# Kernel tuning notes

Measured on AMD Instinct MI355X. Metric: run time of the kernel, lower is better.

## Reference

```python
import jax, jax.numpy as jnp
import numpy as np

H = 16          # num heads
DH = 64         # head size
D = H * DH      # hidden size 1024
B, S = 2, 2048


def setup_inputs() -> dict:
    key = jax.random.key(0)
    ks = jax.random.split(key, 9)
    scale = 1.0 / np.sqrt(D)
    p = {}
    p["hidden_states"] = jax.random.normal(ks[0], (B, S, D), dtype=jnp.float32)
    for i, name in enumerate(["q", "k", "v", "o"]):
        # stored so that y = x @ W + b (transpose of torch Linear weight)
        p[f"W{name}"] = jax.random.normal(ks[1 + 2 * i], (D, D), dtype=jnp.float32) * scale
        p[f"b{name}"] = jax.random.normal(ks[2 + 2 * i], (D,), dtype=jnp.float32) * 0.01
    return p


def reference(hidden_states, Wq, bq, Wk, bk, Wv, bv, Wo, bo):
    b, s, _ = hidden_states.shape
    q = hidden_states @ Wq + bq  # [B,S,D]
    k = hidden_states @ Wk + bk
    v = hidden_states @ Wv + bv
    # [B,H,S,DH]
    q = q.reshape(b, s, H, DH).transpose(0, 2, 1, 3)
    k = k.reshape(b, s, H, DH).transpose(0, 2, 1, 3)
    v = v.reshape(b, s, H, DH).transpose(0, 2, 1, 3)
    scores = jnp.einsum("bhqd,bhkd->bhqk", q, k) / np.sqrt(DH)
    causal = jnp.triu(jnp.ones((s, s), dtype=bool), k=1)  # True above diagonal -> masked
    scores = jnp.where(causal, -jnp.inf, scores)
    attn = jax.nn.softmax(scores, axis=-1)  # dropout p=0 (eval)
    ctx = jnp.einsum("bhqk,bhkd->bhqd", attn, v)
    ctx = ctx.transpose(0, 2, 1, 3).reshape(b, s, D)
    return ctx @ Wo + bo
```

## Files before the change

kernel.cpp:

```cpp
#include <hip/hip_runtime.h>


typedef _Float16 f16x8 __attribute__((ext_vector_type(8)));
typedef _Float16 f16x4 __attribute__((ext_vector_type(4)));
typedef __fp16 h16x2 __attribute__((ext_vector_type(2)));
typedef float f32x4 __attribute__((ext_vector_type(4)));
typedef float f32x16 __attribute__((ext_vector_type(16)));

#define GLD_LDS16(g, l)                                                        \
  __builtin_amdgcn_global_load_lds(                                            \
      (__attribute__((address_space(1))) const unsigned int*)(g),              \
      (__attribute__((address_space(3))) unsigned int*)(l), 16, 0, 0)

static constexpr int Sdim = 2048;
static constexpr int Ddim = 1024;
static constexpr int NH = 16;
static constexpr int DH = 64;
static constexpr int Mrows = 4096;

static constexpr float QSCALE = 0.125f * 1.44269504f;

__global__ __launch_bounds__(256) void xcvt(const float* __restrict__ X,
                                            _Float16* __restrict__ Y) {
  size_t i = ((size_t)blockIdx.x * 256 + threadIdx.x) * 8;
  float4 f0 = *(const float4*)(X + i);
  float4 f1 = *(const float4*)(X + i + 4);
  alignas(16) _Float16 h[8] = {(_Float16)f0.x, (_Float16)f0.y, (_Float16)f0.z,
                               (_Float16)f0.w, (_Float16)f1.x, (_Float16)f1.y,
                               (_Float16)f1.z, (_Float16)f1.w};
  *(uint4*)(Y + i) = *(const uint4*)h;
}

struct WtArgs {
  const float *s0, *s1, *s2, *s3;
  _Float16 *d0, *d1, *d2, *d3;
};

__global__ __launch_bounds__(256) void wtrans(WtArgs a) {
  __shared__ _Float16 L[64 * 72];
  const int z = blockIdx.z;
  const float* src = z == 0 ? a.s0 : z == 1 ? a.s1 : z == 2 ? a.s2 : a.s3;
  _Float16* dst = z == 0 ? a.d0 : z == 1 ? a.d1 : z == 2 ? a.d2 : a.d3;
  const int k0 = blockIdx.x * 64, n0 = blockIdx.y * 64, t = threadIdx.x;
#pragma unroll
  for (int i = 0; i < 4; ++i) {
    int c = i * 256 + t;
    int row = c >> 4, cc = c & 15;
    float4 f = *(const float4*)&src[(size_t)(k0 + row) * Ddim + n0 + cc * 4];
    L[(cc * 4 + 0) * 72 + row] = (_Float16)f.x;
    L[(cc * 4 + 1) * 72 + row] = (_Float16)f.y;
    L[(cc * 4 + 2) * 72 + row] = (_Float16)f.z;
    L[(cc * 4 + 3) * 72 + row] = (_Float16)f.w;
  }
  __syncthreads();
#pragma unroll
  for (int i = 0; i < 2; ++i) {
    int c = i * 256 + t;
    int n = c >> 3, cc = c & 7;
    *(uint4*)&dst[(size_t)(n0 + n) * Ddim + k0 + cc * 8] =
        *(const uint4*)&L[n * 72 + cc * 8];
  }
}

struct GemmArgs {
  const _Float16* A;
  const _Float16 *Bt0, *Bt1, *Bt2;
  const float *b0, *b1, *b2;
  void *o0, *o1, *o2;
};

template <int MODE>
__global__ __launch_bounds__(256) void gemm128(GemmArgs g) {
  constexpr int K = 1024;
  __shared__ _Float16 As[128 * 32];
  __shared__ _Float16 Bs[128 * 32];
  const int z = blockIdx.z;
  const _Float16* A = g.A;
  const _Float16* Bt = z == 0 ? g.Bt0 : z == 1 ? g.Bt1 : g.Bt2;
  const float* bias = z == 0 ? g.b0 : z == 1 ? g.b1 : g.b2;
  void* out = z == 0 ? g.o0 : z == 1 ? g.o1 : g.o2;
  const int m0 = blockIdx.x * 128, n0 = blockIdx.y * 128;
  const int t = threadIdx.x, lane = t & 63, wv = t >> 6;
  const int wm = wv >> 1, wn = wv & 1, quad = lane >> 4, r = lane & 15;

  const int c0 = wv * 64 + lane, c1 = c0 + 256;
  const _Float16* ga0 = A + (size_t)(m0 + (c0 >> 2)) * K + (c0 & 3) * 8;
  const _Float16* ga1 = A + (size_t)(m0 + (c1 >> 2)) * K + (c1 & 3) * 8;
  const _Float16* gb0 = Bt + (size_t)(n0 + (c0 >> 2)) * K + (c0 & 3) * 8;
  const _Float16* gb1 = Bt + (size_t)(n0 + (c1 >> 2)) * K + (c1 & 3) * 8;
  char* lA0 = (char*)As + (wv * 64) * 16;
  char* lA1 = (char*)As + (256 + wv * 64) * 16;
  char* lB0 = (char*)Bs + (wv * 64) * 16;
  char* lB1 = (char*)Bs + (256 + wv * 64) * 16;

  f32x4 acc[4][4] = {};
  for (int kt = 0; kt < K; kt += 32) {
    GLD_LDS16(ga0 + kt, lA0);
    GLD_LDS16(ga1 + kt, lA1);
    GLD_LDS16(gb0 + kt, lB0);
    GLD_LDS16(gb1 + kt, lB1);
    __syncthreads();
    f16x8 af[4], bf[4];
#pragma unroll
    for (int mi = 0; mi < 4; ++mi)
      af[mi] = *(const f16x8*)&As[(wm * 64 + mi * 16 + r) * 32 + quad * 8];
#pragma unroll
    for (int ni = 0; ni < 4; ++ni)
      bf[ni] = *(const f16x8*)&Bs[(wn * 64 + ni * 16 + r) * 32 + quad * 8];
#pragma unroll
    for (int mi = 0; mi < 4; ++mi)
#pragma unroll
      for (int ni = 0; ni < 4; ++ni)
        acc[mi][ni] = __builtin_amdgcn_mfma_f32_16x16x32_f16(af[mi], bf[ni],
                                                             acc[mi][ni], 0, 0, 0);
    __syncthreads();
  }

  const float scale = (MODE == 0 && z == 0) ? QSCALE : 1.0f;
  float bv[4];
#pragma unroll
  for (int ni = 0; ni < 4; ++ni) bv[ni] = bias[n0 + wn * 64 + ni * 16 + r];
#pragma unroll
  for (int mi = 0; mi < 4; ++mi) {
#pragma unroll
    for (int ni = 0; ni < 4; ++ni) {
      const int n = n0 + wn * 64 + ni * 16 + r;
      if (MODE == 0 && z == 2) {
        alignas(8) _Float16 h4[4];
#pragma unroll
        for (int reg = 0; reg < 4; ++reg)
          h4[reg] = (_Float16)(acc[mi][ni][reg] + bv[ni]);
        const int m = m0 + wm * 64 + mi * 16 + quad * 4;
        const int b = m >> 11, s = m & 2047, h = n >> 6, dh = n & 63;
        *(uint2*)&((_Float16*)out)[((size_t)(b * NH + h) * DH + dh) * Sdim + s] =
            *(const uint2*)h4;
      } else {
#pragma unroll
        for (int reg = 0; reg < 4; ++reg) {
          const int m = m0 + wm * 64 + mi * 16 + quad * 4 + reg;
          const float v = (acc[mi][ni][reg] + bv[ni]) * scale;
          if (MODE == 0) {
            const int b = m >> 11, s = m & 2047, h = n >> 6, dh = n & 63;
            ((_Float16*)out)[(((size_t)(b * NH + h) * Sdim + s) << 6) + dh] =
                (_Float16)v;
          } else {
            ((float*)out)[(size_t)m * Ddim + n] = v;
          }
        }
      }
    }
  }
}

__global__ __launch_bounds__(256) void attn(const _Float16* __restrict__ Q,
                                            const _Float16* __restrict__ Kk,
                                            const _Float16* __restrict__ Vt,
                                            _Float16* __restrict__ ctx) {
  __shared__ _Float16 Ks[2][64 * 64], Vs[2][64 * 64];
  const int id = blockIdx.x, xcd = id & 7, slot = id >> 3;
  const int qt = 31 - (slot >> 2);
  const int bh = ((slot & 3) << 3) | xcd;
  const int q0 = qt * 64;
  const int t = threadIdx.x, lane = t & 63, wv = t >> 6;
  const int qh = wv & 1, kvh = wv >> 1;
  const int n31 = lane & 31, h5 = lane >> 5, h8 = h5 * 8;
  const int b = bh >> 4, h = bh & 15;
  const _Float16* Kg = Kk + (size_t)bh * Sdim * DH;
  const _Float16* Vg = Vt + (size_t)bh * DH * Sdim;

  const int qg = q0 + qh * 32 + n31;
  const _Float16* Qrow = Q + ((size_t)bh * Sdim + qg) * DH;
  f16x8 aq[4];
#pragma unroll
  for (int ks = 0; ks < 4; ++ks) aq[ks] = *(const f16x8*)(Qrow + ks * 16 + h8);

  const int ntiles = qt + 1;
  const int sr = t >> 3, sr2 = sr + 32, sc = (t & 7) * 8;
  const int kr = (sr & 51) | ((sr & 4) << 1) | ((sr & 8) >> 1);
  const int kr2 = (sr2 & 51) | ((sr2 & 4) << 1) | ((sr2 & 8) >> 1);
  const int kc = sc ^ ((kr & 7) << 3), kc2 = sc ^ ((kr2 & 7) << 3);
  const int vc = sc ^ ((sr & 7) << 3), vc2 = sc ^ ((sr2 & 7) << 3);

  f32x16 oacc0 = {}, oacc1 = {};
  float l_i = 0.f;

  uint4 ka = *(const uint4*)&Kg[(size_t)sr * DH + sc];
  uint4 kb = *(const uint4*)&Kg[(size_t)sr2 * DH + sc];
  uint4 va = *(const uint4*)&Vg[(size_t)sr * Sdim + sc];
  uint4 vb = *(const uint4*)&Vg[(size_t)sr2 * Sdim + sc];
  *(uint4*)&Ks[0][kr * 64 + kc] = ka;
  *(uint4*)&Ks[0][kr2 * 64 + kc2] = kb;
  *(uint4*)&Vs[0][sr * 64 + vc] = va;
  *(uint4*)&Vs[0][sr2 * 64 + vc2] = vb;

  const int prow = kvh * 32 + n31;
  const int pb = prow * 64, psw = (prow & 7) << 3;
  const int vsw = (n31 & 7) << 3;

  for (int it = 0; it < ntiles; ++it) {
    const int cur = it & 1;
    if (it + 1 < ntiles) {
      const int kvn = (it + 1) * 64;
      ka = *(const uint4*)&Kg[(size_t)(kvn + sr) * DH + sc];
      kb = *(const uint4*)&Kg[(size_t)(kvn + sr2) * DH + sc];
      va = *(const uint4*)&Vg[(size_t)sr * Sdim + kvn + sc];
      vb = *(const uint4*)&Vg[(size_t)sr2 * Sdim + kvn + sc];
    }
    __syncthreads();

    f32x16 sacc = {};
    __builtin_amdgcn_s_setprio(1);
#pragma unroll
    for (int ks = 0; ks < 4; ++ks) {
      f16x8 ak = *(const f16x8*)&Ks[cur][pb + ((ks * 16 + h8) ^ psw)];
      sacc = __builtin_amdgcn_mfma_f32_32x32x16_f16(ak, aq[ks], sacc, 0, 0, 0);
    }
    __builtin_amdgcn_s_setprio(0);

    const int kvb = it * 64;
    if (it == ntiles - 1) {
#pragma unroll
      for (int i = 0; i < 16; ++i) {
        const int kvgl = kvb + kvh * 32 + (i & 7) + h8 + 16 * (i >> 3);
        if (kvgl > qg) sacc[i] = -1e30f;
      }
    }
#pragma unroll
    for (int i = 0; i < 16; ++i) {
      const float p = exp2f(sacc[i]);
      l_i += p;
      sacc[i] = p;
    }
    union U { f16x8 v8; h16x2 v2[4]; } u0, u1;
#pragma unroll
    for (int i = 0; i < 4; ++i) {
      u0.v2[i] = __builtin_amdgcn_cvt_pkrtz(sacc[2 * i], sacc[2 * i + 1]);
      u1.v2[i] = __builtin_amdgcn_cvt_pkrtz(sacc[8 + 2 * i], sacc[9 + 2 * i]);
    }

    __builtin_amdgcn_s_setprio(1);
#pragma unroll
    for (int ks = 0; ks < 2; ++ks) {
      const f16x8 ap = ks ? u1.v8 : u0.v8;
      const int col = kvh * 32 + ks * 16 + h8;
      f16x8 bv0 = *(const f16x8*)&Vs[cur][n31 * 64 + (col ^ vsw)];
      f16x8 bv1 = *(const f16x8*)&Vs[cur][(32 + n31) * 64 + (col ^ vsw)];
      oacc0 = __builtin_amdgcn_mfma_f32_32x32x16_f16(ap, bv0, oacc0, 0, 0, 0);
      oacc1 = __builtin_amdgcn_mfma_f32_32x32x16_f16(ap, bv1, oacc1, 0, 0, 0);
    }
    __builtin_amdgcn_s_setprio(0);

    if (it + 1 < ntiles) {
      const int nxt = cur ^ 1;
      *(uint4*)&Ks[nxt][kr * 64 + kc] = ka;
      *(uint4*)&Ks[nxt][kr2 * 64 + kc2] = kb;
      *(uint4*)&Vs[nxt][sr * 64 + vc] = va;
      *(uint4*)&Vs[nxt][sr2 * 64 + vc2] = vb;
    }
  }

  l_i += __shfl_xor(l_i, 32, 64);
  __syncthreads();
  float* obuf = (float*)&Ks[0][0] + qh * (64 * 32);
  float* lbuf = (float*)&Vs[0][0] + qh * 64;
  union V16 { f32x16 v; f32x4 q[4]; };
  if (kvh == 1) {
    V16 a, c;
    a.v = oacc0;
    c.v = oacc1;
#pragma unroll
    for (int k = 0; k < 4; ++k) {
      *(f32x4*)&obuf[lane * 32 + ((k ^ (lane & 7)) << 2)] = a.q[k];
      *(f32x4*)&obuf[lane * 32 + (((k + 4) ^ (lane & 7)) << 2)] = c.q[k];
    }
    lbuf[lane] = l_i;
  }
  __syncthreads();
  if (kvh == 0) {
    V16 a, c;
#pragma unroll
    for (int k = 0; k < 4; ++k) {
      a.q[k] = *(const f32x4*)&obuf[lane * 32 + ((k ^ (lane & 7)) << 2)];
      c.q[k] = *(const f32x4*)&obuf[lane * 32 + (((k + 4) ^ (lane & 7)) << 2)];
    }
    oacc0 += a.v;
    oacc1 += c.v;
    l_i += lbuf[lane];
#pragma unroll
    for (int rr = 0; rr < 16; ++rr) {
      const int qrow = (rr & 3) + 8 * (rr >> 2) + 4 * h5;
      const float rl = 1.0f / __shfl(l_i, qrow, 64);
      const int s = q0 + qh * 32 + qrow;
      const size_t base = ((size_t)b * Sdim + s) * Ddim + h * DH;
      ctx[base + n31] = (_Float16)(oacc0[rr] * rl);
      ctx[base + 32 + n31] = (_Float16)(oacc1[rr] * rl);
    }
  }
}

extern "C" void kernel_launch(void* const* d_in, const int* in_sizes, int n_in,
                              void* d_out, int out_size, void* d_ws,
                              size_t ws_size, hipStream_t stream) {
  const float* hid = (const float*)d_in[0];
  const float* Wq = (const float*)d_in[1];
  const float* bq = (const float*)d_in[2];
  const float* Wk = (const float*)d_in[3];
  const float* bk = (const float*)d_in[4];
  const float* Wv = (const float*)d_in[5];
  const float* bv = (const float*)d_in[6];
  const float* Wo = (const float*)d_in[7];
  const float* bo = (const float*)d_in[8];

  char* ws = (char*)d_ws;
  _Float16* Xh = (_Float16*)(ws);
  _Float16* Wqt = (_Float16*)(ws + (8ull << 20));
  _Float16* Wkt = (_Float16*)(ws + (10ull << 20));
  _Float16* Wvt = (_Float16*)(ws + (12ull << 20));
  _Float16* Wot = (_Float16*)(ws + (14ull << 20));
  _Float16* Qb = (_Float16*)(ws + (16ull << 20));
  _Float16* Kb = (_Float16*)(ws + (24ull << 20));
  _Float16* Vtb = (_Float16*)(ws + (32ull << 20));
  _Float16* ctx = Xh;

  xcvt<<<dim3(Mrows * Ddim / (256 * 8)), 256, 0, stream>>>(hid, Xh);

  WtArgs wa{Wq, Wk, Wv, Wo, Wqt, Wkt, Wvt, Wot};
  wtrans<<<dim3(16, 16, 4), 256, 0, stream>>>(wa);

  GemmArgs g1{Xh, Wqt, Wkt, Wvt, bq, bk, bv, Qb, Kb, Vtb};
  gemm128<0><<<dim3(Mrows / 128, Ddim / 128, 3), 256, 0, stream>>>(g1);

  attn<<<dim3(1024), 256, 0, stream>>>(Qb, Kb, Vtb, ctx);

  GemmArgs g2{ctx, Wot, Wot, Wot, bo, bo, bo, d_out, d_out, d_out};
  gemm128<1><<<dim3(Mrows / 128, Ddim / 128, 1), 256, 0, stream>>>(g2);
}
```

Before: 184.4 us.

## Merge prep kernels, narrow output GEMM tile, split QK MFMA accumulator chain

Merges the input-cast and weight-transpose kernels into one launch, saving a kernel launch and its gap. Templates the GEMM on tile width and runs the output projection with 64-wide N tiles, doubling its grid from 256 to 512 blocks for better CU occupancy. In attention, splits the QK^T MFMA chain into two independent accumulators summed afterwards, shortening the dependent MFMA latency chain at the cost of extra registers.

```diff
diff --git a/kernel.cpp b/kernel.cpp
--- a/kernel.cpp
+++ b/kernel.cpp
@@ -20,28 +20,30 @@
 
 static constexpr float QSCALE = 0.125f * 1.44269504f;
 
-__global__ __launch_bounds__(256) void xcvt(const float* __restrict__ X,
-                                            _Float16* __restrict__ Y) {
-  size_t i = ((size_t)blockIdx.x * 256 + threadIdx.x) * 8;
-  float4 f0 = *(const float4*)(X + i);
-  float4 f1 = *(const float4*)(X + i + 4);
-  alignas(16) _Float16 h[8] = {(_Float16)f0.x, (_Float16)f0.y, (_Float16)f0.z,
-                               (_Float16)f0.w, (_Float16)f1.x, (_Float16)f1.y,
-                               (_Float16)f1.z, (_Float16)f1.w};
-  *(uint4*)(Y + i) = *(const uint4*)h;
-}
-
-struct WtArgs {
+struct PrepArgs {
+  const float* X;
+  _Float16* Y;
   const float *s0, *s1, *s2, *s3;
   _Float16 *d0, *d1, *d2, *d3;
 };
 
-__global__ __launch_bounds__(256) void wtrans(WtArgs a) {
+__global__ __launch_bounds__(256) void prep(PrepArgs a) {
   __shared__ _Float16 L[64 * 72];
-  const int z = blockIdx.z;
+  const int id = blockIdx.x, t = threadIdx.x;
+  if (id >= 1024) {
+    size_t i = ((size_t)(id - 1024) * 256 + t) * 8;
+    float4 f0 = *(const float4*)(a.X + i);
+    float4 f1 = *(const float4*)(a.X + i + 4);
+    alignas(16) _Float16 h[8] = {(_Float16)f0.x, (_Float16)f0.y, (_Float16)f0.z,
+                                 (_Float16)f0.w, (_Float16)f1.x, (_Float16)f1.y,
+                                 (_Float16)f1.z, (_Float16)f1.w};
+    *(uint4*)(a.Y + i) = *(const uint4*)h;
+    return;
+  }
+  const int z = id >> 8;
   const float* src = z == 0 ? a.s0 : z == 1 ? a.s1 : z == 2 ? a.s2 : a.s3;
   _Float16* dst = z == 0 ? a.d0 : z == 1 ? a.d1 : z == 2 ? a.d2 : a.d3;
-  const int k0 = blockIdx.x * 64, n0 = blockIdx.y * 64, t = threadIdx.x;
+  const int k0 = (id & 15) * 64, n0 = ((id >> 4) & 15) * 64;
 #pragma unroll
   for (int i = 0; i < 4; ++i) {
     int c = i * 256 + t;
@@ -69,17 +71,19 @@
   void *o0, *o1, *o2;
 };
 
-template <int MODE>
-__global__ __launch_bounds__(256) void gemm128(GemmArgs g) {
+template <int MODE, int BN>
+__global__ __launch_bounds__(256) void gemmT(GemmArgs g) {
   constexpr int K = 1024;
+  constexpr int WN = BN / 2;
+  constexpr int NI = WN / 16;
   __shared__ _Float16 As[128 * 32];
-  __shared__ _Float16 Bs[128 * 32];
+  __shared__ _Float16 Bs[BN * 32];
   const int z = blockIdx.z;
   const _Float16* A = g.A;
   const _Float16* Bt = z == 0 ? g.Bt0 : z == 1 ? g.Bt1 : g.Bt2;
   const float* bias = z == 0 ? g.b0 : z == 1 ? g.b1 : g.b2;
   void* out = z == 0 ? g.o0 : z == 1 ? g.o1 : g.o2;
-  const int m0 = blockIdx.x * 128, n0 = blockIdx.y * 128;
+  const int m0 = blockIdx.x * 128, n0 = blockIdx.y * BN;
   const int t = threadIdx.x, lane = t & 63, wv = t >> 6;
   const int wm = wv >> 1, wn = wv & 1, quad = lane >> 4, r = lane & 15;
 
@@ -87,44 +91,45 @@
   const _Float16* ga0 = A + (size_t)(m0 + (c0 >> 2)) * K + (c0 & 3) * 8;
   const _Float16* ga1 = A + (size_t)(m0 + (c1 >> 2)) * K + (c1 & 3) * 8;
   const _Float16* gb0 = Bt + (size_t)(n0 + (c0 >> 2)) * K + (c0 & 3) * 8;
-  const _Float16* gb1 = Bt + (size_t)(n0 + (c1 >> 2)) * K + (c1 & 3) * 8;
+  const _Float16* gb1 =
+      Bt + (size_t)(n0 + ((c1 >> 2) & (BN - 1))) * K + (c1 & 3) * 8;
   char* lA0 = (char*)As + (wv * 64) * 16;
   char* lA1 = (char*)As + (256 + wv * 64) * 16;
   char* lB0 = (char*)Bs + (wv * 64) * 16;
   char* lB1 = (char*)Bs + (256 + wv * 64) * 16;
 
-  f32x4 acc[4][4] = {};
+  f32x4 acc[4][NI] = {};
   for (int kt = 0; kt < K; kt += 32) {
     GLD_LDS16(ga0 + kt, lA0);
     GLD_LDS16(ga1 + kt, lA1);
     GLD_LDS16(gb0 + kt, lB0);
-    GLD_LDS16(gb1 + kt, lB1);
+    if constexpr (BN == 128) GLD_LDS16(gb1 + kt, lB1);
     __syncthreads();
-    f16x8 af[4], bf[4];
+    f16x8 af[4], bf[NI];
 #pragma unroll
     for (int mi = 0; mi < 4; ++mi)
       af[mi] = *(const f16x8*)&As[(wm * 64 + mi * 16 + r) * 32 + quad * 8];
 #pragma unroll
-    for (int ni = 0; ni < 4; ++ni)
-      bf[ni] = *(const f16x8*)&Bs[(wn * 64 + ni * 16 + r) * 32 + quad * 8];
+    for (int ni = 0; ni < NI; ++ni)
+      bf[ni] = *(const f16x8*)&Bs[(wn * WN + ni * 16 + r) * 32 + quad * 8];
 #pragma unroll
     for (int mi = 0; mi < 4; ++mi)
 #pragma unroll
-      for (int ni = 0; ni < 4; ++ni)
+      for (int ni = 0; ni < NI; ++ni)
         acc[mi][ni] = __builtin_amdgcn_mfma_f32_16x16x32_f16(af[mi], bf[ni],
                                                              acc[mi][ni], 0, 0, 0);
     __syncthreads();
   }
 
   const float scale = (MODE == 0 && z == 0) ? QSCALE : 1.0f;
-  float bv[4];
-#pragma unroll
-  for (int ni = 0; ni < 4; ++ni) bv[ni] = bias[n0 + wn * 64 + ni * 16 + r];
+  float bv[NI];
+#pragma unroll
+  for (int ni = 0; ni < NI; ++ni) bv[ni] = bias[n0 + wn * WN + ni * 16 + r];
 #pragma unroll
   for (int mi = 0; mi < 4; ++mi) {
 #pragma unroll
-    for (int ni = 0; ni < 4; ++ni) {
-      const int n = n0 + wn * 64 + ni * 16 + r;
+    for (int ni = 0; ni < NI; ++ni) {
+      const int n = n0 + wn * WN + ni * 16 + r;
       if (MODE == 0 && z == 2) {
         alignas(8) _Float16 h4[4];
 #pragma unroll
@@ -208,14 +213,17 @@
     }
     __syncthreads();
 
-    f32x16 sacc = {};
+    f32x16 sa = {}, sb = {};
     __builtin_amdgcn_s_setprio(1);
 #pragma unroll
-    for (int ks = 0; ks < 4; ++ks) {
-      f16x8 ak = *(const f16x8*)&Ks[cur][pb + ((ks * 16 + h8) ^ psw)];
-      sacc = __builtin_amdgcn_mfma_f32_32x32x16_f16(ak, aq[ks], sacc, 0, 0, 0);
+    for (int ks = 0; ks < 2; ++ks) {
+      f16x8 ak0 = *(const f16x8*)&Ks[cur][pb + ((ks * 16 + h8) ^ psw)];
+      f16x8 ak1 = *(const f16x8*)&Ks[cur][pb + (((ks + 2) * 16 + h8) ^ psw)];
+      sa = __builtin_amdgcn_mfma_f32_32x32x16_f16(ak0, aq[ks], sa, 0, 0, 0);
+      sb = __builtin_amdgcn_mfma_f32_32x32x16_f16(ak1, aq[ks + 2], sb, 0, 0, 0);
     }
     __builtin_amdgcn_s_setprio(0);
+    f32x16 sacc = sa + sb;
 
     const int kvb = it * 64;
     if (it == ntiles - 1) {
@@ -322,16 +330,14 @@
   _Float16* Vtb = (_Float16*)(ws + (32ull << 20));
   _Float16* ctx = Xh;
 
-  xcvt<<<dim3(Mrows * Ddim / (256 * 8)), 256, 0, stream>>>(hid, Xh);
-
-  WtArgs wa{Wq, Wk, Wv, Wo, Wqt, Wkt, Wvt, Wot};
-  wtrans<<<dim3(16, 16, 4), 256, 0, stream>>>(wa);
+  PrepArgs pa{hid, Xh, Wq, Wk, Wv, Wo, Wqt, Wkt, Wvt, Wot};
+  prep<<<dim3(3072), 256, 0, stream>>>(pa);
 
   GemmArgs g1{Xh, Wqt, Wkt, Wvt, bq, bk, bv, Qb, Kb, Vtb};
-  gemm128<0><<<dim3(Mrows / 128, Ddim / 128, 3), 256, 0, stream>>>(g1);
+  gemmT<0, 128><<<dim3(Mrows / 128, Ddim / 128, 3), 256, 0, stream>>>(g1);
 
   attn<<<dim3(1024), 256, 0, stream>>>(Qb, Kb, Vtb, ctx);
 
   GemmArgs g2{ctx, Wot, Wot, Wot, bo, bo, bo, d_out, d_out, d_out};
-  gemm128<1><<<dim3(Mrows / 128, Ddim / 128, 1), 256, 0, stream>>>(g2);
+  gemmT<1, 64><<<dim3(Mrows / 128, Ddim / 64, 1), 256, 0, stream>>>(g2);
 }
```

Result: faster. 180.0 us (-2.3%).
